# Kernel optimization log

Measured on AMD Instinct MI355X. Metric: run time of the kernel, lower is better.

The kernel has to match this reference:

```python
import jax, jax.numpy as jnp
import numpy as np

N_NODES = 100000
N_EDGES = 1600000
D_FEAT = 128
HIDDEN = 128
HEADS = 4
OUT_C = HIDDEN // HEADS  # 32
N_CLASSES = 10
N_GRAPHS = 64
NEG_SLOPE = 0.2


def glorot(key, shape, fan_in, fan_out):
    s = jnp.sqrt(6.0 / (fan_in + fan_out))
    return jax.random.uniform(key, shape, minval=-s, maxval=s, dtype=jnp.float32)


def setup_inputs() -> dict:
    key = jax.random.key(0)
    ks = jax.random.split(key, 24)
    x = jax.random.normal(ks[0], (N_NODES, D_FEAT), dtype=jnp.float32)
    src = jax.random.randint(ks[1], (N_EDGES,), 0, N_NODES, dtype=jnp.int32)
    off = jax.random.randint(ks[2], (N_EDGES,), 1, N_NODES, dtype=jnp.int32)
    dst = ((src + off) % N_NODES).astype(jnp.int32)  # guarantees no self-loops
    edge_index = jnp.stack([src, dst], axis=0)
    batch = jnp.sort(jax.random.randint(ks[3], (N_NODES,), 0, N_GRAPHS, dtype=jnp.int32))
    inp = {"x": x, "edge_index": edge_index, "batch": batch}
    # GATConv layer params: W [in, H*C] (lin_l == lin_r), att_l/att_r [H, C], bias [H*C]
    ins = [D_FEAT, HIDDEN, HIDDEN]
    for i in range(3):
        k = 4 + 4 * i
        inp[f"W{i+1}"] = glorot(ks[k], (ins[i], HEADS * OUT_C), ins[i], HEADS * OUT_C)
        inp[f"al{i+1}"] = glorot(ks[k + 1], (HEADS, OUT_C), HEADS * OUT_C, 1)
        inp[f"ar{i+1}"] = glorot(ks[k + 2], (HEADS, OUT_C), HEADS * OUT_C, 1)
        inp[f"b{i+1}"] = jnp.zeros((HEADS * OUT_C,), jnp.float32)
    inp["lin1_w"] = glorot(ks[16], (HIDDEN, HIDDEN), HIDDEN, HIDDEN)
    inp["lin1_b"] = jnp.zeros((HIDDEN,), jnp.float32)
    inp["lin2_w"] = glorot(ks[17], (HIDDEN, N_CLASSES), HIDDEN, N_CLASSES)
    inp["lin2_b"] = jnp.zeros((N_CLASSES,), jnp.float32)
    return inp


def gat_layer(x, src, dst, W, att_l, att_r, bias):
    n = x.shape[0]
    H, C = att_l.shape
    xw = (x @ W).reshape(n, H, C)                       # Theta x
    al = jnp.einsum('nhc,hc->nh', xw, att_l)
    ar = jnp.einsum('nhc,hc->nh', xw, att_r)
    loop = jnp.arange(n, dtype=src.dtype)
    s = jnp.concatenate([src, loop])                    # add self-loops
    d = jnp.concatenate([dst, loop])
    logits = jax.nn.leaky_relu(al[s] + ar[d], NEG_SLOPE)  # [E+N, H]
    m = jax.ops.segment_max(logits, d, num_segments=n)    # segment softmax over dst
    e = jnp.exp(logits - m[d])
    z = jax.ops.segment_sum(e, d, num_segments=n)
    alpha = e / z[d]
    msg = xw[s] * alpha[:, :, None]                     # [E+N, H, C]
    out = jax.ops.segment_sum(msg, d, num_segments=n)   # scatter-add aggregate
    return out.reshape(n, H * C) + bias


def reference(x, edge_index, batch,
              W1, al1, ar1, b1, W2, al2, ar2, b2, W3, al3, ar3, b3,
              lin1_w, lin1_b, lin2_w, lin2_b):
    src, dst = edge_index[0], edge_index[1]
    h = jax.nn.relu(gat_layer(x, src, dst, W1, al1, ar1, b1))
    h = jax.nn.relu(gat_layer(h, src, dst, W2, al2, ar2, b2))
    h = jax.nn.relu(gat_layer(h, src, dst, W3, al3, ar3, b3))
    last = h
    # global mean pool over graphs in the batch
    s = jax.ops.segment_sum(h, batch, num_segments=N_GRAPHS)
    cnt = jax.ops.segment_sum(jnp.ones((h.shape[0],), h.dtype), batch, num_segments=N_GRAPHS)
    pooled = s / jnp.maximum(cnt, 1.0)[:, None]
    g = jax.nn.relu(pooled @ lin1_w + lin1_b)           # dropout inactive (eval)
    logits = g @ lin2_w + lin2_b
    return (jax.nn.log_softmax(logits, axis=-1), last)
```

## Files before the change

### kernel.cpp

```cpp
#include <hip/hip_runtime.h>
#include <math.h>


#define LRELU(x) ((x) > 0.f ? (x) : 0.2f*(x))
#define SH 7
#define TILE 4096
#define EPT 16

typedef __attribute__((ext_vector_type(8))) short s16x8;
typedef __attribute__((ext_vector_type(4))) float f32x4;

__device__ inline unsigned short f2bf(float f){
  unsigned u = __float_as_uint(f);
  u += 0x7fff + ((u >> 16) & 1);
  return (unsigned short)(u >> 16);
}

__global__ __launch_bounds__(256) void k_bcnt(const int* __restrict__ dst,
    int* __restrict__ bcnt, int E, int NB){
  __shared__ int lh[1024];
  int t = threadIdx.x;
  for (int j = t; j < 1024; j += 256) lh[j] = 0;
  __syncthreads();
  int base = blockIdx.x * TILE;
  int lim = min(base + TILE, E);
  for (int e = base + t; e < lim; e += 256)
    atomicAdd(&lh[dst[e] >> SH], 1);
  __syncthreads();
  for (int j = t; j < NB; j += 256){
    int v = lh[j];
    if (v) atomicAdd(&bcnt[j], v);
  }
}

__global__ __launch_bounds__(256) void k_bscan(const int* __restrict__ bcnt,
    int* __restrict__ bstart, int* __restrict__ bfill, int NB, int E){
  __shared__ int c[1024];
  __shared__ int ps[256];
  int t = threadIdx.x;
  for (int j = t; j < 1024; j += 256) c[j] = (j < NB) ? bcnt[j] : 0;
  __syncthreads();
  int b0 = 4*t;
  int v0=c[b0], v1=c[b0+1], v2=c[b0+2], v3=c[b0+3];
  int e1=v0, e2=v0+v1, e3=e2+v2, ts=e3+v3;
  ps[t] = ts; __syncthreads();
  for (int off=1; off<256; off<<=1){
    int x = (t>=off) ? ps[t-off] : 0; __syncthreads();
    ps[t] += x; __syncthreads();
  }
  int pre = ps[t] - ts;
  int ex0=pre, ex1=pre+e1, ex2=pre+e2, ex3=pre+e3;
  if (b0   < NB){ bstart[b0]=ex0;   bfill[b0]=ex0; }
  if (b0+1 < NB){ bstart[b0+1]=ex1; bfill[b0+1]=ex1; }
  if (b0+2 < NB){ bstart[b0+2]=ex2; bfill[b0+2]=ex2; }
  if (b0+3 < NB){ bstart[b0+3]=ex3; bfill[b0+3]=ex3; }
  if (t == 0) bstart[NB] = E;
}

__global__ __launch_bounds__(256) void k_part(const int* __restrict__ src,
    const int* __restrict__ dst, int* __restrict__ bfill,
    int2* __restrict__ tmp, int E){
  __shared__ int2 reorder[TILE];
  __shared__ int lhist[1024], lscan[1024], lgbase[1024];
  __shared__ int ps[256];
  int t = threadIdx.x;
  int tb = blockIdx.x * TILE;
  int tilecnt = min(TILE, E - tb);
  for (int j = t; j < 1024; j += 256) lhist[j] = 0;
  __syncthreads();
  int ss[EPT], dd[EPT], rk[EPT];
  #pragma unroll
  for (int i = 0; i < EPT; i++){
    int e = tb + t + i*256;
    if (e < E){
      ss[i] = src[e]; dd[i] = dst[e];
      rk[i] = atomicAdd(&lhist[dd[i] >> SH], 1);
    }
  }
  __syncthreads();
  int b0 = 4*t;
  int v0=lhist[b0], v1=lhist[b0+1], v2=lhist[b0+2], v3=lhist[b0+3];
  int e1=v0, e2=v0+v1, e3=e2+v2, ts=e3+v3;
  ps[t] = ts; __syncthreads();
  for (int off=1; off<256; off<<=1){
    int x = (t>=off) ? ps[t-off] : 0; __syncthreads();
    ps[t] += x; __syncthreads();
  }
  int pre = ps[t] - ts;
  int ex[4] = {pre, pre+e1, pre+e2, pre+e3};
  lscan[b0]=ex[0]; lscan[b0+1]=ex[1]; lscan[b0+2]=ex[2]; lscan[b0+3]=ex[3];
  int cb[4] = {v0, v1, v2, v3};
  #pragma unroll
  for (int i = 0; i < 4; i++){
    if (cb[i] > 0){
      int gb = atomicAdd(&bfill[b0+i], cb[i]);
      lgbase[b0+i] = gb - ex[i];
    }
  }
  __syncthreads();
  #pragma unroll
  for (int i = 0; i < EPT; i++){
    int e = tb + t + i*256;
    if (e < E){
      int b = dd[i] >> SH;
      reorder[lscan[b] + rk[i]] = make_int2(ss[i], dd[i]);
    }
  }
  __syncthreads();
  for (int j = t; j < tilecnt; j += 256){
    int2 p = reorder[j];
    tmp[lgbase[p.y >> SH] + j] = p;
  }
}

__global__ __launch_bounds__(256) void k_csr(const int2* __restrict__ tmp,
    const int* __restrict__ bstart, int* __restrict__ rp, int* __restrict__ col,
    int n, int E){
  __shared__ int lcnt[128];
  __shared__ int sc[128];
  int b = blockIdx.x, t = threadIdx.x;
  int node0 = b << SH;
  int ncnt = min(128, n - node0);
  int be = bstart[b], ee = bstart[b+1];
  if (t < 128) lcnt[t] = 0;
  __syncthreads();
  for (int e = be + t; e < ee; e += 256)
    atomicAdd(&lcnt[tmp[e].y - node0], 1);
  __syncthreads();
  int v = (t < 128) ? lcnt[t] : 0;
  if (t < 128) sc[t] = v;
  __syncthreads();
  for (int off=1; off<128; off<<=1){
    int x = 0;
    if (t < 128 && t >= off) x = sc[t-off];
    __syncthreads();
    if (t < 128) sc[t] += x;
    __syncthreads();
  }
  if (t < 128){
    int start = be + sc[t] - v;
    lcnt[t] = start;
    if (t < ncnt) rp[node0 + t] = start;
  }
  if (t == 0 && node0 + ncnt == n) rp[n] = E;
  __syncthreads();
  for (int e = be + t; e < ee; e += 256){
    int2 p = tmp[e];
    int pos = atomicAdd(&lcnt[p.y - node0], 1);
    col[pos] = p.x;
  }
}

__global__ void k_bounds(const int* __restrict__ batch, int* __restrict__ gstart, int n){
  int g = threadIdx.x;
  if (g > 64) return;
  int lo = 0, hi = n;
  while (lo < hi){
    int mid = (lo + hi) >> 1;
    if (batch[mid] < g) lo = mid + 1; else hi = mid;
  }
  gstart[g] = lo;
}

template<bool BF16IN>
__global__ __launch_bounds__(256) void k_gemm(
    const void* __restrict__ Xv, const float* __restrict__ W,
    const float* __restrict__ attl, const float* __restrict__ attr,
    unsigned short* __restrict__ XW, float* __restrict__ AL, float* __restrict__ AR, int n)
{
  __shared__ unsigned short Wt[128*128];
  __shared__ unsigned short Xl[64*136];
  int t = threadIdx.x;
  int lane = t & 63, w = t >> 6;
  int l15 = lane & 15, quad = lane >> 4;
  for (int i = 0; i < 64; i++){
    int e = i*256 + t;
    int k = e >> 7, nn = e & 127;
    Wt[nn*128 + ((((k>>3) ^ (nn&15))<<3) | (k&7))] = f2bf(W[e]);
  }
  int ntiles = (n + 63) >> 6;
  int r_ = t >> 2, seg = t & 3;
  for (int tile = blockIdx.x; tile < ntiles; tile += gridDim.x){
    int row0 = tile << 6;
    __syncthreads();
    {
      int grow = row0 + r_;
      unsigned short* dp = &Xl[r_*136 + seg*32];
      if (grow < n){
        if (BF16IN){
          const uint4* gp = (const uint4*)((const unsigned short*)Xv + (size_t)grow*128 + seg*32);
          #pragma unroll
          for (int i = 0; i < 4; i++) ((uint4*)dp)[i] = gp[i];
        } else {
          const float4* gp = (const float4*)((const float*)Xv + (size_t)grow*128 + seg*32);
          #pragma unroll
          for (int i = 0; i < 8; i++){
            float4 v = gp[i];
            ((unsigned*)dp)[i*2]   = (unsigned)f2bf(v.x) | ((unsigned)f2bf(v.y) << 16);
            ((unsigned*)dp)[i*2+1] = (unsigned)f2bf(v.z) | ((unsigned)f2bf(v.w) << 16);
          }
        }
      } else {
        #pragma unroll
        for (int i = 0; i < 4; i++) ((uint4*)dp)[i] = make_uint4(0,0,0,0);
      }
    }
    __syncthreads();
    f32x4 acc[4][2];
    #pragma unroll
    for (int rt = 0; rt < 4; rt++){ acc[rt][0] = (f32x4){0,0,0,0}; acc[rt][1] = (f32x4){0,0,0,0}; }
    #pragma unroll
    for (int ks = 0; ks < 4; ks++){
      s16x8 b0 = *(const s16x8*)&Wt[(w*32 + l15)*128      + (((ks*4+quad) ^ l15)<<3)];
      s16x8 b1 = *(const s16x8*)&Wt[(w*32 + 16 + l15)*128 + (((ks*4+quad) ^ l15)<<3)];
      #pragma unroll
      for (int rt = 0; rt < 4; rt++){
        s16x8 a = *(const s16x8*)&Xl[(rt*16 + l15)*136 + ks*32 + quad*8];
        acc[rt][0] = __builtin_amdgcn_mfma_f32_16x16x32_bf16(a, b0, acc[rt][0], 0, 0, 0);
        acc[rt][1] = __builtin_amdgcn_mfma_f32_16x16x32_bf16(a, b1, acc[rt][1], 0, 0, 0);
      }
    }
    __syncthreads();
    #pragma unroll
    for (int rt = 0; rt < 4; rt++)
      #pragma unroll
      for (int c2 = 0; c2 < 2; c2++)
        #pragma unroll
        for (int r = 0; r < 4; r++)
          Xl[(rt*16 + quad*4 + r)*136 + w*32 + c2*16 + l15] = f2bf(acc[rt][c2][r]);
    __syncthreads();
    {
      int grow = row0 + r_;
      if (grow < n){
        const unsigned short* sp = &Xl[r_*136 + seg*32];
        uint4 uu[4];
        #pragma unroll
        for (int i = 0; i < 4; i++) uu[i] = ((const uint4*)sp)[i];
        unsigned short* gx = XW + (size_t)grow*128 + seg*32;
        #pragma unroll
        for (int i = 0; i < 4; i++) ((uint4*)gx)[i] = uu[i];
        const unsigned* up = (const unsigned*)uu;
        const float4* alp = (const float4*)(attl + seg*32);
        const float4* arp = (const float4*)(attr + seg*32);
        float pl = 0.f, pr = 0.f;
        #pragma unroll
        for (int i = 0; i < 8; i++){
          unsigned ua = up[i*2], ub = up[i*2+1];
          float x0 = __uint_as_float(ua << 16);
          float x1 = __uint_as_float(ua & 0xffff0000u);
          float x2 = __uint_as_float(ub << 16);
          float x3 = __uint_as_float(ub & 0xffff0000u);
          float4 av = alp[i];
          float4 rv = arp[i];
          pl += x0*av.x + x1*av.y + x2*av.z + x3*av.w;
          pr += x0*rv.x + x1*rv.y + x2*rv.z + x3*rv.w;
        }
        AL[grow*4 + seg] = pl;
        AR[grow*4 + seg] = pr;
      }
    }
  }
}

template<bool BF16OUT>
__global__ __launch_bounds__(256) void k_attn(
    const unsigned short* __restrict__ XW, const float* __restrict__ AL, const float* __restrict__ AR,
    const int* __restrict__ rp, const int* __restrict__ col,
    const float* __restrict__ bias, void* __restrict__ OUT, int n)
{
  __shared__ float ebuf[4][64*4];
  __shared__ int   sbuf[4][64];
  int wv = threadIdx.x >> 6;
  int d = blockIdx.x*4 + wv;
  int lane = threadIdx.x & 63;
  if (d >= n) return;
  int start = rp[d], end = rp[d+1];
  float4 ald4 = ((const float4*)AL)[d];
  float4 ard4 = ((const float4*)AR)[d];
  float ar0 = ard4.x, ar1 = ard4.y, ar2 = ard4.z, ar3 = ard4.w;
  float es0 = __expf(LRELU(ald4.x + ar0));
  float es1 = __expf(LRELU(ald4.y + ar1));
  float es2 = __expf(LRELU(ald4.z + ar2));
  float es3 = __expf(LRELU(ald4.w + ar3));
  int h = lane >> 4;
  float eself = h==0?es0 : h==1?es1 : h==2?es2 : es3;
  const unsigned* XWr = (const unsigned*)XW;
  unsigned v = XWr[(size_t)d*64 + lane];
  float acc0 = eself * __uint_as_float(v << 16);
  float acc1 = eself * __uint_as_float(v & 0xffff0000u);
  float zl0 = 0.f, zl1 = 0.f, zl2 = 0.f, zl3 = 0.f;
  float* eb = ebuf[wv];
  int*   sb = sbuf[wv];
  for (int base = start; base < end; base += 64){
    int cnt = min(64, end - base);
    int s = (lane < cnt) ? col[base + lane] : 0;
    float4 a = ((const float4*)AL)[s];
    float w0 = __expf(LRELU(a.x + ar0));
    float w1 = __expf(LRELU(a.y + ar1));
    float w2 = __expf(LRELU(a.z + ar2));
    float w3 = __expf(LRELU(a.w + ar3));
    if (lane >= cnt){ w0 = w1 = w2 = w3 = 0.f; }
    zl0 += w0; zl1 += w1; zl2 += w2; zl3 += w3;
    float4 w4; w4.x = w0; w4.y = w1; w4.z = w2; w4.w = w3;
    ((float4*)eb)[lane] = w4;
    sb[lane] = s;
    #pragma unroll 4
    for (int j = 0; j < cnt; j++){
      int sj = sb[j];
      float w = eb[j*4 + h];
      unsigned u = XWr[(size_t)sj*64 + lane];
      acc0 = fmaf(w, __uint_as_float(u << 16), acc0);
      acc1 = fmaf(w, __uint_as_float(u & 0xffff0000u), acc1);
    }
  }
  #pragma unroll
  for (int off = 32; off >= 1; off >>= 1){
    zl0 += __shfl_xor(zl0, off, 64);
    zl1 += __shfl_xor(zl1, off, 64);
    zl2 += __shfl_xor(zl2, off, 64);
    zl3 += __shfl_xor(zl3, off, 64);
  }
  float z_h = (h==0?zl0 : h==1?zl1 : h==2?zl2 : zl3) + eself;
  float rz = 1.f / z_h;
  int ch = lane*2;
  float o0 = fmaf(acc0, rz, bias[ch]);
  float o1 = fmaf(acc1, rz, bias[ch+1]);
  o0 = o0 > 0.f ? o0 : 0.f;
  o1 = o1 > 0.f ? o1 : 0.f;
  if (BF16OUT){
    unsigned pk = (unsigned)f2bf(o0) | ((unsigned)f2bf(o1) << 16);
    ((unsigned*)OUT)[(size_t)d*64 + lane] = pk;
  } else {
    float2 o; o.x = o0; o.y = o1;
    ((float2*)OUT)[(size_t)d*64 + lane] = o;
  }
}

__global__ __launch_bounds__(128) void k_pool(const float* __restrict__ H,
                                              const int* __restrict__ gstart,
                                              float* __restrict__ psum){
  int g = blockIdx.x >> 3, slice = blockIdx.x & 7, t = threadIdx.x;
  int s0 = gstart[g], s1 = gstart[g+1];
  int cntg = s1 - s0;
  int chunk = (cntg + 7) >> 3;
  int lo = s0 + slice*chunk;
  int hi = min(lo + chunk, s1);
  float sum = 0.f;
  for (int i = lo; i < hi; i++) sum += H[(size_t)i*128 + t];
  atomicAdd(&psum[g*128 + t], sum);
}

__global__ __launch_bounds__(128) void k_mlp(const float* __restrict__ psum,
                       const int* __restrict__ gstart,
                       const float* __restrict__ w1, const float* __restrict__ b1,
                       const float* __restrict__ w2, const float* __restrict__ b2,
                       float* __restrict__ out)
{
  __shared__ float p[128];
  __shared__ float gsh[128];
  __shared__ float lg[10];
  int g = blockIdx.x, t = threadIdx.x;
  float c = fmaxf((float)(gstart[g+1] - gstart[g]), 1.f);
  p[t] = psum[g*128 + t] / c;
  __syncthreads();
  float acc = b1[t];
  for (int k = 0; k < 128; k++) acc = fmaf(p[k], w1[k*128 + t], acc);
  gsh[t] = acc > 0.f ? acc : 0.f;
  __syncthreads();
  if (t < 10){
    float a = b2[t];
    for (int k = 0; k < 128; k++) a = fmaf(gsh[k], w2[k*10 + t], a);
    lg[t] = a;
  }
  __syncthreads();
  if (t < 10){
    float mx = lg[0];
    for (int c2 = 1; c2 < 10; c2++) mx = fmaxf(mx, lg[c2]);
    float se = 0.f;
    for (int c2 = 0; c2 < 10; c2++) se += __expf(lg[c2] - mx);
    out[g*10 + t] = lg[t] - mx - logf(se);
  }
}

extern "C" void kernel_launch(void* const* d_in, const int* in_sizes, int n_in,
                              void* d_out, int out_size, void* d_ws, size_t ws_size,
                              hipStream_t stream)
{
  const float* x    = (const float*)d_in[0];
  const int* eidx   = (const int*)d_in[1];
  const int* batch  = (const int*)d_in[2];
  const float* W[3]  = {(const float*)d_in[3], (const float*)d_in[7],  (const float*)d_in[11]};
  const float* al[3] = {(const float*)d_in[4], (const float*)d_in[8],  (const float*)d_in[12]};
  const float* ar[3] = {(const float*)d_in[5], (const float*)d_in[9],  (const float*)d_in[13]};
  const float* bs[3] = {(const float*)d_in[6], (const float*)d_in[10], (const float*)d_in[14]};
  const float* l1w = (const float*)d_in[15];
  const float* l1b = (const float*)d_in[16];
  const float* l2w = (const float*)d_in[17];
  const float* l2b = (const float*)d_in[18];
  int E = in_sizes[1] / 2;
  int n = in_sizes[2];
  const int* srcp = eidx;
  const int* dstp = eidx + E;
  int NB = (n + 127) >> SH;

  char* wsp = (char*)d_ws;
  auto alloc = [&](size_t bytes){ void* p = (void*)wsp; wsp += (bytes + 255) & ~(size_t)255; return p; };
  unsigned short* xw   = (unsigned short*)alloc((size_t)n*128*2);
  unsigned short* hbuf = (unsigned short*)alloc((size_t)n*128*2);
  float* ALb  = (float*)alloc((size_t)n*4*4);
  float* ARb  = (float*)alloc((size_t)n*4*4);
  int* rp     = (int*)alloc((size_t)(n+1)*4);
  int* col    = (int*)alloc((size_t)E*4);
  int2* tmp   = (int2*)alloc((size_t)E*8);
  int* bcnt   = (int*)alloc(1024*4);
  int* bstart = (int*)alloc(1025*4);
  int* bfill  = (int*)alloc(1024*4);
  float* psum = (float*)alloc(64*128*4);
  int* gstart = (int*)alloc(65*4);

  float* outlog = (float*)d_out;
  float* h3     = (float*)d_out + 64*10;

  hipMemsetAsync(bcnt, 0, 1024*4,   stream);
  hipMemsetAsync(psum, 0, 64*128*4, stream);

  int nparts = (E + TILE - 1) / TILE;
  k_bcnt <<<nparts, 256, 0, stream>>>(dstp, bcnt, E, NB);
  k_bscan<<<1, 256, 0, stream>>>(bcnt, bstart, bfill, NB, E);
  k_part <<<nparts, 256, 0, stream>>>(srcp, dstp, bfill, tmp, E);
  k_csr  <<<NB, 256, 0, stream>>>(tmp, bstart, rp, col, n, E);

  k_bounds<<<1, 128, 0, stream>>>(batch, gstart, n);

  const int GG = 768;
  k_gemm<false><<<GG, 256, 0, stream>>>(x, W[0], al[0], ar[0], xw, ALb, ARb, n);
  k_attn<true><<<(n+3)/4, 256, 0, stream>>>(xw, ALb, ARb, rp, col, bs[0], hbuf, n);
  k_gemm<true><<<GG, 256, 0, stream>>>(hbuf, W[1], al[1], ar[1], xw, ALb, ARb, n);
  k_attn<true><<<(n+3)/4, 256, 0, stream>>>(xw, ALb, ARb, rp, col, bs[1], hbuf, n);
  k_gemm<true><<<GG, 256, 0, stream>>>(hbuf, W[2], al[2], ar[2], xw, ALb, ARb, n);
  k_attn<false><<<(n+3)/4, 256, 0, stream>>>(xw, ALb, ARb, rp, col, bs[2], h3, n);

  k_pool<<<64*8, 128, 0, stream>>>(h3, gstart, psum);
  k_mlp <<<64, 128, 0, stream>>>(psum, gstart, l1w, l1b, l2w, l2b, outlog);
}
```

Measured before the change: 599.8 us.

## Fuse CSR bucket histogram with first GEMM and merge small setup kernels

Runs the destination-bucket histogram blocks and the first-layer GEMM in one launch, folds the graph-boundary search into the bucket scan, and replaces two memsets with a small init kernel, cutting launch count and serial gaps. Bucket width doubles to 256 nodes, which halves the bucket count and changes the scan and CSR kernels to match. The attention kernel now uses 32-bit pre-shifted row indices with deeper unrolling. The coarser buckets put more edges per CSR block, and the fused launch makes histogram blocks compete with GEMM blocks for the same GPU.

After: 580.9 us. -3.2%, faster.

```diff
diff --git a/kernel.cpp b/kernel.cpp
--- a/kernel.cpp
+++ b/kernel.cpp
@@ -3,7 +3,7 @@
 
 
 #define LRELU(x) ((x) > 0.f ? (x) : 0.2f*(x))
-#define SH 7
+#define SH 8
 #define TILE 4096
 #define EPT 16
 
@@ -16,160 +16,20 @@
   return (unsigned short)(u >> 16);
 }
 
-__global__ __launch_bounds__(256) void k_bcnt(const int* __restrict__ dst,
-    int* __restrict__ bcnt, int E, int NB){
-  __shared__ int lh[1024];
+__global__ void k_init(int* __restrict__ bcnt, float* __restrict__ psum){
   int t = threadIdx.x;
-  for (int j = t; j < 1024; j += 256) lh[j] = 0;
-  __syncthreads();
-  int base = blockIdx.x * TILE;
-  int lim = min(base + TILE, E);
-  for (int e = base + t; e < lim; e += 256)
-    atomicAdd(&lh[dst[e] >> SH], 1);
-  __syncthreads();
-  for (int j = t; j < NB; j += 256){
-    int v = lh[j];
-    if (v) atomicAdd(&bcnt[j], v);
-  }
-}
-
-__global__ __launch_bounds__(256) void k_bscan(const int* __restrict__ bcnt,
-    int* __restrict__ bstart, int* __restrict__ bfill, int NB, int E){
-  __shared__ int c[1024];
-  __shared__ int ps[256];
-  int t = threadIdx.x;
-  for (int j = t; j < 1024; j += 256) c[j] = (j < NB) ? bcnt[j] : 0;
-  __syncthreads();
-  int b0 = 4*t;
-  int v0=c[b0], v1=c[b0+1], v2=c[b0+2], v3=c[b0+3];
-  int e1=v0, e2=v0+v1, e3=e2+v2, ts=e3+v3;
-  ps[t] = ts; __syncthreads();
-  for (int off=1; off<256; off<<=1){
-    int x = (t>=off) ? ps[t-off] : 0; __syncthreads();
-    ps[t] += x; __syncthreads();
-  }
-  int pre = ps[t] - ts;
-  int ex0=pre, ex1=pre+e1, ex2=pre+e2, ex3=pre+e3;
-  if (b0   < NB){ bstart[b0]=ex0;   bfill[b0]=ex0; }
-  if (b0+1 < NB){ bstart[b0+1]=ex1; bfill[b0+1]=ex1; }
-  if (b0+2 < NB){ bstart[b0+2]=ex2; bfill[b0+2]=ex2; }
-  if (b0+3 < NB){ bstart[b0+3]=ex3; bfill[b0+3]=ex3; }
-  if (t == 0) bstart[NB] = E;
-}
-
-__global__ __launch_bounds__(256) void k_part(const int* __restrict__ src,
-    const int* __restrict__ dst, int* __restrict__ bfill,
-    int2* __restrict__ tmp, int E){
-  __shared__ int2 reorder[TILE];
-  __shared__ int lhist[1024], lscan[1024], lgbase[1024];
-  __shared__ int ps[256];
-  int t = threadIdx.x;
-  int tb = blockIdx.x * TILE;
-  int tilecnt = min(TILE, E - tb);
-  for (int j = t; j < 1024; j += 256) lhist[j] = 0;
-  __syncthreads();
-  int ss[EPT], dd[EPT], rk[EPT];
-  #pragma unroll
-  for (int i = 0; i < EPT; i++){
-    int e = tb + t + i*256;
-    if (e < E){
-      ss[i] = src[e]; dd[i] = dst[e];
-      rk[i] = atomicAdd(&lhist[dd[i] >> SH], 1);
-    }
-  }
-  __syncthreads();
-  int b0 = 4*t;
-  int v0=lhist[b0], v1=lhist[b0+1], v2=lhist[b0+2], v3=lhist[b0+3];
-  int e1=v0, e2=v0+v1, e3=e2+v2, ts=e3+v3;
-  ps[t] = ts; __syncthreads();
-  for (int off=1; off<256; off<<=1){
-    int x = (t>=off) ? ps[t-off] : 0; __syncthreads();
-    ps[t] += x; __syncthreads();
-  }
-  int pre = ps[t] - ts;
-  int ex[4] = {pre, pre+e1, pre+e2, pre+e3};
-  lscan[b0]=ex[0]; lscan[b0+1]=ex[1]; lscan[b0+2]=ex[2]; lscan[b0+3]=ex[3];
-  int cb[4] = {v0, v1, v2, v3};
-  #pragma unroll
-  for (int i = 0; i < 4; i++){
-    if (cb[i] > 0){
-      int gb = atomicAdd(&bfill[b0+i], cb[i]);
-      lgbase[b0+i] = gb - ex[i];
-    }
-  }
-  __syncthreads();
-  #pragma unroll
-  for (int i = 0; i < EPT; i++){
-    int e = tb + t + i*256;
-    if (e < E){
-      int b = dd[i] >> SH;
-      reorder[lscan[b] + rk[i]] = make_int2(ss[i], dd[i]);
-    }
-  }
-  __syncthreads();
-  for (int j = t; j < tilecnt; j += 256){
-    int2 p = reorder[j];
-    tmp[lgbase[p.y >> SH] + j] = p;
-  }
-}
-
-__global__ __launch_bounds__(256) void k_csr(const int2* __restrict__ tmp,
-    const int* __restrict__ bstart, int* __restrict__ rp, int* __restrict__ col,
-    int n, int E){
-  __shared__ int lcnt[128];
-  __shared__ int sc[128];
-  int b = blockIdx.x, t = threadIdx.x;
-  int node0 = b << SH;
-  int ncnt = min(128, n - node0);
-  int be = bstart[b], ee = bstart[b+1];
-  if (t < 128) lcnt[t] = 0;
-  __syncthreads();
-  for (int e = be + t; e < ee; e += 256)
-    atomicAdd(&lcnt[tmp[e].y - node0], 1);
-  __syncthreads();
-  int v = (t < 128) ? lcnt[t] : 0;
-  if (t < 128) sc[t] = v;
-  __syncthreads();
-  for (int off=1; off<128; off<<=1){
-    int x = 0;
-    if (t < 128 && t >= off) x = sc[t-off];
-    __syncthreads();
-    if (t < 128) sc[t] += x;
-    __syncthreads();
-  }
-  if (t < 128){
-    int start = be + sc[t] - v;
-    lcnt[t] = start;
-    if (t < ncnt) rp[node0 + t] = start;
-  }
-  if (t == 0 && node0 + ncnt == n) rp[n] = E;
-  __syncthreads();
-  for (int e = be + t; e < ee; e += 256){
-    int2 p = tmp[e];
-    int pos = atomicAdd(&lcnt[p.y - node0], 1);
-    col[pos] = p.x;
-  }
-}
-
-__global__ void k_bounds(const int* __restrict__ batch, int* __restrict__ gstart, int n){
-  int g = threadIdx.x;
-  if (g > 64) return;
-  int lo = 0, hi = n;
-  while (lo < hi){
-    int mid = (lo + hi) >> 1;
-    if (batch[mid] < g) lo = mid + 1; else hi = mid;
-  }
-  gstart[g] = lo;
+  bcnt[t] = 0; bcnt[256 + t] = 0;
+  for (int i = t; i < 8192; i += 256) psum[i] = 0.f;
 }
 
 template<bool BF16IN>
-__global__ __launch_bounds__(256) void k_gemm(
+__device__ __forceinline__ void gemm_body(
+    unsigned short* Wt, unsigned short* Xl,
     const void* __restrict__ Xv, const float* __restrict__ W,
     const float* __restrict__ attl, const float* __restrict__ attr,
-    unsigned short* __restrict__ XW, float* __restrict__ AL, float* __restrict__ AR, int n)
-{
-  __shared__ unsigned short Wt[128*128];
-  __shared__ unsigned short Xl[64*136];
+    unsigned short* __restrict__ XW, float* __restrict__ AL, float* __restrict__ AR,
+    int n, int bid, int gstride)
+{
   int t = threadIdx.x;
   int lane = t & 63, w = t >> 6;
   int l15 = lane & 15, quad = lane >> 4;
@@ -180,7 +40,7 @@
   }
   int ntiles = (n + 63) >> 6;
   int r_ = t >> 2, seg = t & 3;
-  for (int tile = blockIdx.x; tile < ntiles; tile += gridDim.x){
+  for (int tile = bid; tile < ntiles; tile += gstride){
     int row0 = tile << 6;
     __syncthreads();
     {
@@ -262,6 +122,163 @@
   }
 }
 
+template<bool BF16IN>
+__global__ __launch_bounds__(256) void k_gemm(
+    const void* __restrict__ Xv, const float* __restrict__ W,
+    const float* __restrict__ attl, const float* __restrict__ attr,
+    unsigned short* __restrict__ XW, float* __restrict__ AL, float* __restrict__ AR, int n)
+{
+  __shared__ unsigned short Wt[128*128];
+  __shared__ unsigned short Xl[64*136];
+  gemm_body<BF16IN>(Wt, Xl, Xv, W, attl, attr, XW, AL, AR, n, blockIdx.x, gridDim.x);
+}
+
+__global__ __launch_bounds__(256) void k_fuse1(
+    const int* __restrict__ dst, int* __restrict__ bcnt, int E, int nparts,
+    const float* __restrict__ X, const float* __restrict__ W,
+    const float* __restrict__ attl, const float* __restrict__ attr,
+    unsigned short* __restrict__ XW, float* __restrict__ AL, float* __restrict__ AR, int n)
+{
+  __shared__ unsigned short Wt[128*128];
+  __shared__ unsigned short Xl[64*136];
+  if ((int)blockIdx.x < nparts){
+    int* lh = (int*)Wt;
+    int t = threadIdx.x;
+    for (int j = t; j < 512; j += 256) lh[j] = 0;
+    __syncthreads();
+    int base = blockIdx.x * TILE;
+    int lim = min(base + TILE, E);
+    for (int e = base + t; e < lim; e += 256)
+      atomicAdd(&lh[dst[e] >> SH], 1);
+    __syncthreads();
+    for (int j = t; j < 512; j += 256){
+      int v = lh[j];
+      if (v) atomicAdd(&bcnt[j], v);
+    }
+    return;
+  }
+  gemm_body<false>(Wt, Xl, X, W, attl, attr, XW, AL, AR, n,
+                   (int)blockIdx.x - nparts, (int)gridDim.x - nparts);
+}
+
+__global__ __launch_bounds__(256) void k_bscan(const int* __restrict__ bcnt,
+    int* __restrict__ bstart, int* __restrict__ bfill, int NB, int E,
+    const int* __restrict__ batch, int* __restrict__ gstart, int n){
+  int t = threadIdx.x;
+  if (blockIdx.x == 1){
+    int g = t;
+    if (g > 64) return;
+    int lo = 0, hi = n;
+    while (lo < hi){
+      int mid = (lo + hi) >> 1;
+      if (batch[mid] < g) lo = mid + 1; else hi = mid;
+    }
+    gstart[g] = lo;
+    return;
+  }
+  __shared__ int c[512];
+  __shared__ int ps[256];
+  for (int j = t; j < 512; j += 256) c[j] = (j < NB) ? bcnt[j] : 0;
+  __syncthreads();
+  int b0 = 2*t;
+  int v0 = c[b0], v1 = c[b0+1];
+  int ts = v0 + v1;
+  ps[t] = ts; __syncthreads();
+  for (int off = 1; off < 256; off <<= 1){
+    int x = (t >= off) ? ps[t-off] : 0; __syncthreads();
+    ps[t] += x; __syncthreads();
+  }
+  int pre = ps[t] - ts;
+  if (b0   < NB){ bstart[b0]   = pre;    bfill[b0]   = pre; }
+  if (b0+1 < NB){ bstart[b0+1] = pre+v0; bfill[b0+1] = pre+v0; }
+  if (t == 0) bstart[NB] = E;
+}
+
+__global__ __launch_bounds__(256) void k_part(const int* __restrict__ src,
+    const int* __restrict__ dst, int* __restrict__ bfill,
+    int2* __restrict__ tmp, int E){
+  __shared__ int2 reorder[TILE];
+  __shared__ int lhist[512], lscan[512], lgbase[512];
+  __shared__ int ps[256];
+  int t = threadIdx.x;
+  int tb = blockIdx.x * TILE;
+  int tilecnt = min(TILE, E - tb);
+  for (int j = t; j < 512; j += 256) lhist[j] = 0;
+  __syncthreads();
+  int ss[EPT], dd[EPT], rk[EPT];
+  #pragma unroll
+  for (int i = 0; i < EPT; i++){
+    int e = tb + t + i*256;
+    if (e < E){
+      ss[i] = src[e]; dd[i] = dst[e];
+      rk[i] = atomicAdd(&lhist[dd[i] >> SH], 1);
+    }
+  }
+  __syncthreads();
+  int b0 = 2*t;
+  int v0 = lhist[b0], v1 = lhist[b0+1];
+  int ts = v0 + v1;
+  ps[t] = ts; __syncthreads();
+  for (int off = 1; off < 256; off <<= 1){
+    int x = (t >= off) ? ps[t-off] : 0; __syncthreads();
+    ps[t] += x; __syncthreads();
+  }
+  int pre = ps[t] - ts;
+  int ex0 = pre, ex1 = pre + v0;
+  lscan[b0] = ex0; lscan[b0+1] = ex1;
+  if (v0 > 0){ int gb = atomicAdd(&bfill[b0],   v0); lgbase[b0]   = gb - ex0; }
+  if (v1 > 0){ int gb = atomicAdd(&bfill[b0+1], v1); lgbase[b0+1] = gb - ex1; }
+  __syncthreads();
+  #pragma unroll
+  for (int i = 0; i < EPT; i++){
+    int e = tb + t + i*256;
+    if (e < E){
+      int b = dd[i] >> SH;
+      reorder[lscan[b] + rk[i]] = make_int2(ss[i], dd[i]);
+    }
+  }
+  __syncthreads();
+  for (int j = t; j < tilecnt; j += 256){
+    int2 p = reorder[j];
+    tmp[lgbase[p.y >> SH] + j] = p;
+  }
+}
+
+__global__ __launch_bounds__(256) void k_csr(const int2* __restrict__ tmp,
+    const int* __restrict__ bstart, int* __restrict__ rp, int* __restrict__ col,
+    int n, int E){
+  __shared__ int lcnt[256];
+  __shared__ int sc[256];
+  int b = blockIdx.x, t = threadIdx.x;
+  int node0 = b << SH;
+  int ncnt = min(256, n - node0);
+  int be = bstart[b], ee = bstart[b+1];
+  lcnt[t] = 0;
+  __syncthreads();
+  for (int e = be + t; e < ee; e += 256)
+    atomicAdd(&lcnt[tmp[e].y - node0], 1);
+  __syncthreads();
+  int v = lcnt[t];
+  sc[t] = v;
+  __syncthreads();
+  for (int off = 1; off < 256; off <<= 1){
+    int x = (t >= off) ? sc[t-off] : 0;
+    __syncthreads();
+    sc[t] += x;
+    __syncthreads();
+  }
+  int start = be + sc[t] - v;
+  lcnt[t] = start;
+  if (t < ncnt) rp[node0 + t] = start;
+  if (t == 0 && node0 + ncnt == n) rp[n] = E;
+  __syncthreads();
+  for (int e = be + t; e < ee; e += 256){
+    int2 p = tmp[e];
+    int pos = atomicAdd(&lcnt[p.y - node0], 1);
+    col[pos] = p.x;
+  }
+}
+
 template<bool BF16OUT>
 __global__ __launch_bounds__(256) void k_attn(
     const unsigned short* __restrict__ XW, const float* __restrict__ AL, const float* __restrict__ AR,
@@ -285,7 +302,7 @@
   int h = lane >> 4;
   float eself = h==0?es0 : h==1?es1 : h==2?es2 : es3;
   const unsigned* XWr = (const unsigned*)XW;
-  unsigned v = XWr[(size_t)d*64 + lane];
+  unsigned v = XWr[(unsigned)d*64 + lane];
   float acc0 = eself * __uint_as_float(v << 16);
   float acc1 = eself * __uint_as_float(v & 0xffff0000u);
   float zl0 = 0.f, zl1 = 0.f, zl2 = 0.f, zl3 = 0.f;
@@ -303,12 +320,12 @@
     zl0 += w0; zl1 += w1; zl2 += w2; zl3 += w3;
     float4 w4; w4.x = w0; w4.y = w1; w4.z = w2; w4.w = w3;
     ((float4*)eb)[lane] = w4;
-    sb[lane] = s;
-    #pragma unroll 4
+    sb[lane] = s << 6;
+    #pragma unroll 8
     for (int j = 0; j < cnt; j++){
-      int sj = sb[j];
+      unsigned sj = (unsigned)sb[j] + lane;
       float w = eb[j*4 + h];
-      unsigned u = XWr[(size_t)sj*64 + lane];
+      unsigned u = XWr[sj];
       acc0 = fmaf(w, __uint_as_float(u << 16), acc0);
       acc1 = fmaf(w, __uint_as_float(u & 0xffff0000u), acc1);
     }
@@ -329,10 +346,10 @@
   o1 = o1 > 0.f ? o1 : 0.f;
   if (BF16OUT){
     unsigned pk = (unsigned)f2bf(o0) | ((unsigned)f2bf(o1) << 16);
-    ((unsigned*)OUT)[(size_t)d*64 + lane] = pk;
+    ((unsigned*)OUT)[(unsigned)d*64 + lane] = pk;
   } else {
     float2 o; o.x = o0; o.y = o1;
-    ((float2*)OUT)[(size_t)d*64 + lane] = o;
+    ((float2*)OUT)[(unsigned)d*64 + lane] = o;
   }
 }
 
@@ -401,7 +418,7 @@
   int n = in_sizes[2];
   const int* srcp = eidx;
   const int* dstp = eidx + E;
-  int NB = (n + 127) >> SH;
+  int NB = (n + 255) >> SH;
 
   char* wsp = (char*)d_ws;
   auto alloc = [&](size_t bytes){ void* p = (void*)wsp; wsp += (bytes + 255) & ~(size_t)255; return p; };
@@ -412,32 +429,28 @@
   int* rp     = (int*)alloc((size_t)(n+1)*4);
   int* col    = (int*)alloc((size_t)E*4);
   int2* tmp   = (int2*)alloc((size_t)E*8);
-  int* bcnt   = (int*)alloc(1024*4);
-  int* bstart = (int*)alloc(1025*4);
-  int* bfill  = (int*)alloc(1024*4);
+  int* bcnt   = (int*)alloc(512*4);
+  int* bstart = (int*)alloc(513*4);
+  int* bfill  = (int*)alloc(512*4);
   float* psum = (float*)alloc(64*128*4);
   int* gstart = (int*)alloc(65*4);
 
   float* outlog = (float*)d_out;
   float* h3     = (float*)d_out + 64*10;
 
-  hipMemsetAsync(bcnt, 0, 1024*4,   stream);
-  hipMemsetAsync(psum, 0, 64*128*4, stream);
-
   int nparts = (E + TILE - 1) / TILE;
-  k_bcnt <<<nparts, 256, 0, stream>>>(dstp, bcnt, E, NB);
-  k_bscan<<<1, 256, 0, stream>>>(bcnt, bstart, bfill, NB, E);
+
+  k_init<<<1, 256, 0, stream>>>(bcnt, psum);
+  k_fuse1<<<nparts + 768, 256, 0, stream>>>(dstp, bcnt, E, nparts,
+                                            x, W[0], al[0], ar[0], xw, ALb, ARb, n);
+  k_bscan<<<2, 256, 0, stream>>>(bcnt, bstart, bfill, NB, E, batch, gstart, n);
   k_part <<<nparts, 256, 0, stream>>>(srcp, dstp, bfill, tmp, E);
   k_csr  <<<NB, 256, 0, stream>>>(tmp, bstart, rp, col, n, E);
 
-  k_bounds<<<1, 128, 0, stream>>>(batch, gstart, n);
-
-  const int GG = 768;
-  k_gemm<false><<<GG, 256, 0, stream>>>(x, W[0], al[0], ar[0], xw, ALb, ARb, n);
   k_attn<true><<<(n+3)/4, 256, 0, stream>>>(xw, ALb, ARb, rp, col, bs[0], hbuf, n);
-  k_gemm<true><<<GG, 256, 0, stream>>>(hbuf, W[1], al[1], ar[1], xw, ALb, ARb, n);
+  k_gemm<true><<<768, 256, 0, stream>>>(hbuf, W[1], al[1], ar[1], xw, ALb, ARb, n);
   k_attn<true><<<(n+3)/4, 256, 0, stream>>>(xw, ALb, ARb, rp, col, bs[1], hbuf, n);
-  k_gemm<true><<<GG, 256, 0, stream>>>(hbuf, W[2], al[2], ar[2], xw, ALb, ARb, n);
+  k_gemm<true><<<768, 256, 0, stream>>>(hbuf, W[2], al[2], ar[2], xw, ALb, ARb, n);
   k_attn<false><<<(n+3)/4, 256, 0, stream>>>(xw, ALb, ARb, rp, col, bs[2], h3, n);
 
   k_pool<<<64*8, 128, 0, stream>>>(h3, gstart, psum);
```
